# Kernel tuning notes

Hardware: AMD Instinct MI355X
Metric: run time of the kernel (lower is better)

The kernel has to match this reference:

```python
import jax, jax.numpy as jnp
import numpy as np

IN_FEATURES = 4096
OUT_FEATURES = 4096


def fht(x):
    """Normalized fast Walsh-Hadamard transform along last axis (n = power of 2).
    Equals x @ H_n / sqrt(n); matches matmul_hadU(t)_cuda when had_K is None (K=1)."""
    n = x.shape[-1]
    orig_shape = x.shape
    x = x.reshape(-1, n)
    h = 1
    while h < n:
        x = x.reshape(-1, n // (2 * h), 2, h)
        a = x[:, :, 0, :]
        b = x[:, :, 1, :]
        x = jnp.stack([a + b, a - b], axis=2).reshape(-1, n)
        h *= 2
    scale = jnp.asarray(1.0 / np.sqrt(n), dtype=x.dtype)
    return (x * scale).reshape(orig_shape)


def decode_e8p(Qidxs, grid_abs):
    """E8P12-style decode: each 16-bit codeword -> 8 fp16 weights.
    Low 8 bits index a 256-entry table of 8 absolute values; high 8 bits are
    per-element sign flips. Returns dense W of shape [out, in]."""
    idx = Qidxs.astype(jnp.int32) & 0xFFFF            # [out, in/8]
    abs_vals = grid_abs[idx & 0xFF]                   # [out, in/8, 8]
    sbits = (idx[..., None] >> (8 + jnp.arange(8, dtype=jnp.int32))) & 1
    signs = (1 - 2 * sbits).astype(grid_abs.dtype)    # [out, in/8, 8] in {+1,-1}
    w = abs_vals * signs
    return w.reshape(Qidxs.shape[0], -1)              # [out, in]


def setup_inputs() -> dict:
    key = jax.random.key(0)
    k1, k2, k3, k4, k5, k6 = jax.random.split(key, 6)
    inp = {}
    inp["input"] = jax.random.normal(k1, (2, 4096, IN_FEATURES), dtype=jnp.float16)
    inp["Qidxs"] = jax.random.randint(k2, (OUT_FEATURES, IN_FEATURES // 8), 0, 65536, dtype=jnp.int32)
    # abs half-integer-ish grid values (E8 lattice magnitudes live in ~[0.25, 3.75])
    inp["grid_abs"] = (jax.random.uniform(k3, (256, 8), dtype=jnp.float32) * 3.0 + 0.25).astype(jnp.float16)
    # SU/SV are random sign vectors in QuIP
    inp["SU"] = (1 - 2 * jax.random.bernoulli(k4, 0.5, (IN_FEATURES,)).astype(jnp.float16))
    inp["SV"] = (1 - 2 * jax.random.bernoulli(k5, 0.5, (OUT_FEATURES,)).astype(jnp.float16))
    inp["Wscale"] = jnp.ones((), dtype=jnp.float32)
    inp["bias"] = jax.random.normal(k6, (OUT_FEATURES,), dtype=jnp.float16) * jnp.float16(0.01)
    return inp


def reference(input, Qidxs, grid_abs, SU, SV, Wscale, bias):
    x = input.reshape(-1, input.shape[-1])            # [T, in]
    x = x * SU                                        # input sign rescale
    x = fht(x)                                        # H^T x / sqrt(n) (H symmetric)
    x = (x * Wscale).astype(jnp.float16)              # global weight scale
    W = decode_e8p(Qidxs, grid_abs)                   # [out, in] dequantized lattice weights
    out = jnp.dot(x, W.T, preferred_element_type=jnp.float32).astype(jnp.float16)  # [T, out]
    out = fht(out)                                    # output Hadamard
    out = out * SV + bias                             # output sign rescale + bias
    return out.reshape(*input.shape[:-1], out.shape[-1])
```

## Files before the change

### kernel.cpp

```cpp
#include <hip/hip_runtime.h>
#include <hip/hip_bf16.h>
#include <stdint.h>

typedef _Float16 f16;
typedef _Float16 f16x8 __attribute__((ext_vector_type(8)));
typedef float f32x4 __attribute__((ext_vector_type(4)));

#define N_FEAT 4096
#define M_ROWS 8192
#define QSTRIDE 512

#define GLD16(gptr, lptr)                                                      \
  __builtin_amdgcn_global_load_lds(                                            \
      (const __attribute__((address_space(1))) void*)(gptr),                   \
      (__attribute__((address_space(3))) void*)(uint32_t)(uintptr_t)(lptr),    \
      16, 0, 0)

#define PADI(i) ((i) + ((i) >> 4))

__device__ __forceinline__ void fht16(float v[16]) {
#pragma unroll
  for (int h = 1; h < 16; h <<= 1) {
#pragma unroll
    for (int i = 0; i < 16; i += (h << 1)) {
#pragma unroll
      for (int j = 0; j < h; ++j) {
        float a = v[i + j], b = v[i + j + h];
        v[i + j] = a + b;
        v[i + j + h] = a - b;
      }
    }
  }
}

__global__ __launch_bounds__(256) void k_fht_in(const float* __restrict__ x,
                                                const float* __restrict__ SU,
                                                const float* __restrict__ wscale,
                                                f16* __restrict__ out) {
  __shared__ float lds[4096 + 256];
  const int row = blockIdx.x;
  const int t = threadIdx.x;
  const float* xr = x + (size_t)row * N_FEAT;
  float v[16];

#pragma unroll
  for (int j = 0; j < 16; ++j) {
    int i = (j << 8) + t;
    v[j] = xr[i] * SU[i];
  }
  fht16(v);
#pragma unroll
  for (int j = 0; j < 16; ++j) lds[PADI((j << 8) + t)] = v[j];
  __syncthreads();

  const int a = t & 15, b = t >> 4;
#pragma unroll
  for (int j = 0; j < 16; ++j) v[j] = lds[PADI((b << 8) + (j << 4) + a)];
  fht16(v);
#pragma unroll
  for (int j = 0; j < 16; ++j) lds[PADI((b << 8) + (j << 4) + a)] = v[j];
  __syncthreads();

#pragma unroll
  for (int j = 0; j < 16; ++j) v[j] = lds[PADI((t << 4) + j)];
  fht16(v);
  const float s = wscale[0] * 0.015625f;
  f16* op = out + (size_t)row * N_FEAT + (t << 4);
  f16x8 o0, o1;
#pragma unroll
  for (int j = 0; j < 8; ++j) {
    o0[j] = (f16)(v[j] * s);
    o1[j] = (f16)(v[j + 8] * s);
  }
  *(f16x8*)(op) = o0;
  *(f16x8*)(op + 8) = o1;
}

__global__ __launch_bounds__(256) void k_decode(const int* __restrict__ q,
                                                const float* __restrict__ grid,
                                                int4* __restrict__ W) {
  __shared__ int4 tab[256];
  const int t = threadIdx.x;
  {
    const float4 g0 = *(const float4*)(grid + t * 8);
    const float4 g1 = *(const float4*)(grid + t * 8 + 4);
    union { f16 h[8]; int4 v; } u;
    u.h[0] = (f16)g0.x; u.h[1] = (f16)g0.y; u.h[2] = (f16)g0.z; u.h[3] = (f16)g0.w;
    u.h[4] = (f16)g1.x; u.h[5] = (f16)g1.y; u.h[6] = (f16)g1.z; u.h[7] = (f16)g1.w;
    tab[t] = u.v;
  }
  __syncthreads();
  const size_t idx = (size_t)blockIdx.x * 256 + t;
  const unsigned c = (unsigned)q[idx] & 0xffffu;
  int4 e = tab[c & 255u];
  e.x ^= (int)((((c >> 8) & 1u) << 15) | (((c >> 9) & 1u) << 31));
  e.y ^= (int)((((c >> 10) & 1u) << 15) | (((c >> 11) & 1u) << 31));
  e.z ^= (int)((((c >> 12) & 1u) << 15) | (((c >> 13) & 1u) << 31));
  e.w ^= (int)((((c >> 14) & 1u) << 15) | (((c >> 15) & 1u) << 31));
  W[idx] = e;
}

#define BM 128
#define BN 128
#define BK 64
#define KDIM 4096

__global__ __launch_bounds__(256) void k_gemm(const f16* __restrict__ A,
                                              const f16* __restrict__ B,
                                              f16* __restrict__ C) {
  __shared__ __attribute__((aligned(16))) f16 sA[BM * BK];
  __shared__ __attribute__((aligned(16))) f16 sB[BN * BK];
  const int tid = threadIdx.x;
  const int lane = tid & 63;
  const int w = tid >> 6;
  const int wr = w >> 1, wc = w & 1;
  const int m0 = blockIdx.y * BM;
  const int n0 = blockIdx.x * BN;

  f32x4 acc[4][4];
#pragma unroll
  for (int i = 0; i < 4; ++i)
#pragma unroll
    for (int j = 0; j < 4; ++j) acc[i][j] = (f32x4)0.0f;

  const int srow = lane >> 3;
  const int scc = lane & 7;
  const int quad = lane >> 4;
  const int ml = lane & 15;

  for (int k0 = 0; k0 < KDIM; k0 += BK) {
#pragma unroll
    for (int i = 0; i < 4; ++i) {
      const int rb = ((w << 2) + i) << 3;
      const int r = rb + srow;
      const int kc = scc ^ (r & 7);
      GLD16(A + (size_t)(m0 + r) * KDIM + k0 + (kc << 3), &sA[rb << 6]);
    }
#pragma unroll
    for (int i = 0; i < 4; ++i) {
      const int rb = ((w << 2) + i) << 3;
      const int r = rb + srow;
      const int kc = scc ^ (r & 7);
      GLD16(B + (size_t)(n0 + r) * KDIM + k0 + (kc << 3), &sB[rb << 6]);
    }
    __syncthreads();

#pragma unroll
    for (int s = 0; s < 2; ++s) {
      f16x8 af[4], bfr[4];
#pragma unroll
      for (int i = 0; i < 4; ++i) {
        const int m = (wr << 6) + (i << 4) + ml;
        const int kc = ((s << 2) + quad) ^ (m & 7);
        af[i] = *(const f16x8*)&sA[(m << 6) + (kc << 3)];
      }
#pragma unroll
      for (int j = 0; j < 4; ++j) {
        const int n = (wc << 6) + (j << 4) + ml;
        const int kc = ((s << 2) + quad) ^ (n & 7);
        bfr[j] = *(const f16x8*)&sB[(n << 6) + (kc << 3)];
      }
#pragma unroll
      for (int i = 0; i < 4; ++i)
#pragma unroll
        for (int j = 0; j < 4; ++j)
          acc[i][j] = __builtin_amdgcn_mfma_f32_16x16x32_f16(af[i], bfr[j],
                                                             acc[i][j], 0, 0, 0);
    }
    __syncthreads();
  }

#pragma unroll
  for (int i = 0; i < 4; ++i) {
#pragma unroll
    for (int j = 0; j < 4; ++j) {
      const int col = n0 + (wc << 6) + (j << 4) + ml;
      const int rowb = m0 + (wr << 6) + (i << 4) + (quad << 2);
#pragma unroll
      for (int r = 0; r < 4; ++r)
        C[(size_t)(rowb + r) * N_FEAT + col] = (f16)acc[i][j][r];
    }
  }
}

__global__ __launch_bounds__(256) void k_fht_out(const f16* __restrict__ Cin,
                                                 const float* __restrict__ SV,
                                                 const float* __restrict__ bias,
                                                 float* __restrict__ out) {
  __shared__ float lds[4096 + 256];
  const int row = blockIdx.x;
  const int t = threadIdx.x;
  const f16* xr = Cin + (size_t)row * N_FEAT;
  float v[16];

#pragma unroll
  for (int j = 0; j < 16; ++j) v[j] = (float)xr[(j << 8) + t];
  fht16(v);
#pragma unroll
  for (int j = 0; j < 16; ++j) lds[PADI((j << 8) + t)] = v[j];
  __syncthreads();

  const int a = t & 15, b = t >> 4;
#pragma unroll
  for (int j = 0; j < 16; ++j) v[j] = lds[PADI((b << 8) + (j << 4) + a)];
  fht16(v);
#pragma unroll
  for (int j = 0; j < 16; ++j) lds[PADI((b << 8) + (j << 4) + a)] = v[j];
  __syncthreads();

#pragma unroll
  for (int j = 0; j < 16; ++j) v[j] = lds[PADI((t << 4) + j)];
  fht16(v);
  float* op = out + (size_t)row * N_FEAT + (t << 4);
  float o[16];
#pragma unroll
  for (int j = 0; j < 16; ++j) {
    int i0 = (t << 4) + j;
    o[j] = v[j] * 0.015625f * SV[i0] + bias[i0];
  }
#pragma unroll
  for (int j = 0; j < 4; ++j)
    *(float4*)(op + 4 * j) = make_float4(o[4 * j], o[4 * j + 1],
                                         o[4 * j + 2], o[4 * j + 3]);
}

extern "C" void kernel_launch(void* const* d_in, const int* in_sizes, int n_in,
                              void* d_out, int out_size, void* d_ws, size_t ws_size,
                              hipStream_t stream) {
  const float* input = nullptr;
  const int* qidxs = nullptr;
  const float* grid_abs = nullptr;
  const float* wscale = nullptr;
  const float* v4k[3] = {nullptr, nullptr, nullptr};
  int n4 = 0;
  for (int i = 0; i < n_in; ++i) {
    switch (in_sizes[i]) {
      case 33554432: input = (const float*)d_in[i]; break;
      case 2097152:  qidxs = (const int*)d_in[i]; break;
      case 2048:     grid_abs = (const float*)d_in[i]; break;
      case 1:        wscale = (const float*)d_in[i]; break;
      case 4096:     if (n4 < 3) v4k[n4++] = (const float*)d_in[i]; break;
      default: break;
    }
  }
  const float* SU = v4k[0];
  const float* SV = v4k[1];
  const float* bias = v4k[2];

  f16* x = (f16*)d_out;
  f16* W = (f16*)((char*)d_out + (size_t)M_ROWS * N_FEAT * 2);
  f16* Cb = (f16*)d_ws;
  float* out = (float*)d_out;

  k_fht_in<<<M_ROWS, 256, 0, stream>>>(input, SU, wscale, x);
  k_decode<<<(N_FEAT * QSTRIDE) / 256, 256, 0, stream>>>(qidxs, grid_abs,
                                                         (int4*)W);
  dim3 g(N_FEAT / BN, M_ROWS / BM);
  k_gemm<<<g, 256, 0, stream>>>(x, W, Cb);
  k_fht_out<<<M_ROWS, 256, 0, stream>>>(Cb, SV, bias, out);
}
```

Measured before the change: 595.4 us.

## Fold output Hadamard into dequantized weights and fuse SV/bias into GEMM epilogue

```diff
diff --git a/kernel.cpp b/kernel.cpp
--- a/kernel.cpp
+++ b/kernel.cpp
@@ -16,7 +16,7 @@
       (__attribute__((address_space(3))) void*)(uint32_t)(uintptr_t)(lptr),    \
       16, 0, 0)
 
-#define PADI(i) ((i) + ((i) >> 4))
+#define PAD64(i) ((i) + (((i) >> 6) << 2))
 
 __device__ __forceinline__ void fht16(float v[16]) {
 #pragma unroll
@@ -31,6 +31,11 @@
       }
     }
   }
+}
+
+__device__ __forceinline__ void fht4(float& a, float& b, float& c, float& d) {
+  float t0 = a + b, t1 = a - b, t2 = c + d, t3 = c - d;
+  a = t0 + t2; b = t1 + t3; c = t0 - t2; d = t1 - t3;
 }
 
 __global__ __launch_bounds__(256) void k_fht_in(const float* __restrict__ x,
@@ -44,60 +49,148 @@
   float v[16];
 
 #pragma unroll
-  for (int j = 0; j < 16; ++j) {
-    int i = (j << 8) + t;
-    v[j] = xr[i] * SU[i];
+  for (int j = 0; j < 4; ++j) {
+    const float4 a = *(const float4*)(xr + (t << 4) + 4 * j);
+    const float4 s = *(const float4*)(SU + (t << 4) + 4 * j);
+    v[4 * j + 0] = a.x * s.x; v[4 * j + 1] = a.y * s.y;
+    v[4 * j + 2] = a.z * s.z; v[4 * j + 3] = a.w * s.w;
   }
   fht16(v);
 #pragma unroll
-  for (int j = 0; j < 16; ++j) lds[PADI((j << 8) + t)] = v[j];
+  for (int j = 0; j < 4; ++j)
+    *(float4*)&lds[PAD64((t << 4) + 4 * j)] =
+        make_float4(v[4 * j], v[4 * j + 1], v[4 * j + 2], v[4 * j + 3]);
   __syncthreads();
 
   const int a = t & 15, b = t >> 4;
 #pragma unroll
-  for (int j = 0; j < 16; ++j) v[j] = lds[PADI((b << 8) + (j << 4) + a)];
+  for (int j = 0; j < 16; ++j) v[j] = lds[PAD64((b << 8) + (j << 4) + a)];
   fht16(v);
 #pragma unroll
-  for (int j = 0; j < 16; ++j) lds[PADI((b << 8) + (j << 4) + a)] = v[j];
-  __syncthreads();
-
-#pragma unroll
-  for (int j = 0; j < 16; ++j) v[j] = lds[PADI((t << 4) + j)];
+  for (int j = 0; j < 16; ++j) lds[PAD64((b << 8) + (j << 4) + a)] = v[j];
+  __syncthreads();
+
+#pragma unroll
+  for (int j = 0; j < 16; ++j) v[j] = lds[PAD64((j << 8) + t)];
   fht16(v);
   const float s = wscale[0] * 0.015625f;
-  f16* op = out + (size_t)row * N_FEAT + (t << 4);
-  f16x8 o0, o1;
-#pragma unroll
-  for (int j = 0; j < 8; ++j) {
-    o0[j] = (f16)(v[j] * s);
-    o1[j] = (f16)(v[j + 8] * s);
-  }
-  *(f16x8*)(op) = o0;
-  *(f16x8*)(op + 8) = o1;
-}
-
-__global__ __launch_bounds__(256) void k_decode(const int* __restrict__ q,
-                                                const float* __restrict__ grid,
-                                                int4* __restrict__ W) {
-  __shared__ int4 tab[256];
+  f16* op = out + (size_t)row * N_FEAT;
+#pragma unroll
+  for (int j = 0; j < 16; ++j) op[(j << 8) + t] = (f16)(v[j] * s);
+}
+
+__global__ __launch_bounds__(256) void k_wA(const int* __restrict__ q,
+                                            const float* __restrict__ grid,
+                                            f16* __restrict__ Wp) {
+  __shared__ float tabf[2048];
+  __shared__ float tile[64 * 65];
   const int t = threadIdx.x;
-  {
-    const float4 g0 = *(const float4*)(grid + t * 8);
-    const float4 g1 = *(const float4*)(grid + t * 8 + 4);
-    union { f16 h[8]; int4 v; } u;
-    u.h[0] = (f16)g0.x; u.h[1] = (f16)g0.y; u.h[2] = (f16)g0.z; u.h[3] = (f16)g0.w;
-    u.h[4] = (f16)g1.x; u.h[5] = (f16)g1.y; u.h[6] = (f16)g1.z; u.h[7] = (f16)g1.w;
-    tab[t] = u.v;
-  }
-  __syncthreads();
-  const size_t idx = (size_t)blockIdx.x * 256 + t;
-  const unsigned c = (unsigned)q[idx] & 0xffffu;
-  int4 e = tab[c & 255u];
-  e.x ^= (int)((((c >> 8) & 1u) << 15) | (((c >> 9) & 1u) << 31));
-  e.y ^= (int)((((c >> 10) & 1u) << 15) | (((c >> 11) & 1u) << 31));
-  e.z ^= (int)((((c >> 12) & 1u) << 15) | (((c >> 13) & 1u) << 31));
-  e.w ^= (int)((((c >> 14) & 1u) << 15) | (((c >> 15) & 1u) << 31));
-  W[idx] = e;
+  const int kg = blockIdx.x;
+  const int ng = blockIdx.y;
+  {
+    *(float4*)&tabf[t * 8] = *(const float4*)(grid + t * 8);
+    *(float4*)&tabf[t * 8 + 4] = *(const float4*)(grid + t * 8 + 4);
+  }
+  __syncthreads();
+
+#pragma unroll
+  for (int e2 = 0; e2 < 2; ++e2) {
+    const int e = t + (e2 << 8);
+    const int nl = e >> 3, c = e & 7;
+    const unsigned code =
+        (unsigned)q[(size_t)(ng * 64 + nl) * QSTRIDE + kg * 8 + c] & 0xffffu;
+    const float* tb = &tabf[(code & 255u) * 8];
+#pragma unroll
+    for (int j = 0; j < 8; ++j) {
+      const int bi = __float_as_int(tb[j]) ^ (int)(((code >> (8 + j)) & 1u) << 31);
+      tile[nl * 65 + (c << 3) + j] = __int_as_float(bi);
+    }
+  }
+  __syncthreads();
+
+  {
+    const int k = t & 63, p = t >> 6;
+    float v[16];
+#pragma unroll
+    for (int j = 0; j < 16; ++j) v[j] = tile[(16 * p + j) * 65 + k];
+    fht16(v);
+#pragma unroll
+    for (int j = 0; j < 16; ++j) tile[(16 * p + j) * 65 + k] = v[j];
+  }
+  __syncthreads();
+
+  {
+    const int k = t & 63, base = (t >> 6) << 2;
+#pragma unroll
+    for (int bb = 0; bb < 4; ++bb) {
+      const int low = base + bb;
+      float v0 = tile[(low) * 65 + k],      v1 = tile[(low + 16) * 65 + k];
+      float v2 = tile[(low + 32) * 65 + k], v3 = tile[(low + 48) * 65 + k];
+      fht4(v0, v1, v2, v3);
+      tile[(low) * 65 + k] = v0;      tile[(low + 16) * 65 + k] = v1;
+      tile[(low + 32) * 65 + k] = v2; tile[(low + 48) * 65 + k] = v3;
+    }
+  }
+  __syncthreads();
+
+  {
+    const int nl = t >> 2, koff = (t & 3) << 4;
+    union { f16 h[16]; int4 v[2]; } u;
+#pragma unroll
+    for (int i = 0; i < 16; ++i) u.h[i] = (f16)tile[nl * 65 + koff + i];
+    int4* dst = (int4*)(Wp + (size_t)(ng * 64 + nl) * N_FEAT + kg * 64 + koff);
+    dst[0] = u.v[0];
+    dst[1] = u.v[1];
+  }
+}
+
+__global__ __launch_bounds__(256) void k_wB(f16* __restrict__ Wp) {
+  __shared__ float tile[64 * 65];
+  const int t = threadIdx.x;
+  const int kg = blockIdx.x;
+  const int n0 = blockIdx.y;
+  {
+    const int n1 = t >> 2, koff = (t & 3) << 4;
+    const f16* src = Wp + (size_t)(n0 + 64 * n1) * N_FEAT + kg * 64 + koff;
+    union { f16 h[16]; int4 v[2]; } u;
+    u.v[0] = ((const int4*)src)[0];
+    u.v[1] = ((const int4*)src)[1];
+#pragma unroll
+    for (int i = 0; i < 16; ++i) tile[n1 * 65 + koff + i] = (float)u.h[i];
+  }
+  __syncthreads();
+  {
+    const int k = t & 63, p = t >> 6;
+    float v[16];
+#pragma unroll
+    for (int j = 0; j < 16; ++j) v[j] = tile[(16 * p + j) * 65 + k];
+    fht16(v);
+#pragma unroll
+    for (int j = 0; j < 16; ++j) tile[(16 * p + j) * 65 + k] = v[j];
+  }
+  __syncthreads();
+  {
+    const int k = t & 63, base = (t >> 6) << 2;
+#pragma unroll
+    for (int bb = 0; bb < 4; ++bb) {
+      const int low = base + bb;
+      float v0 = tile[(low) * 65 + k],      v1 = tile[(low + 16) * 65 + k];
+      float v2 = tile[(low + 32) * 65 + k], v3 = tile[(low + 48) * 65 + k];
+      fht4(v0, v1, v2, v3);
+      tile[(low) * 65 + k] = v0;      tile[(low + 16) * 65 + k] = v1;
+      tile[(low + 32) * 65 + k] = v2; tile[(low + 48) * 65 + k] = v3;
+    }
+  }
+  __syncthreads();
+  {
+    const int n1 = t >> 2, koff = (t & 3) << 4;
+    union { f16 h[16]; int4 v[2]; } u;
+#pragma unroll
+    for (int i = 0; i < 16; ++i) u.h[i] = (f16)tile[n1 * 65 + koff + i];
+    int4* dst = (int4*)(Wp + (size_t)(n0 + 64 * n1) * N_FEAT + kg * 64 + koff);
+    dst[0] = u.v[0];
+    dst[1] = u.v[1];
+  }
 }
 
 #define BM 128
@@ -107,7 +200,9 @@
 
 __global__ __launch_bounds__(256) void k_gemm(const f16* __restrict__ A,
                                               const f16* __restrict__ B,
-                                              f16* __restrict__ C) {
+                                              float* __restrict__ C,
+                                              const float* __restrict__ SV,
+                                              const float* __restrict__ bias) {
   __shared__ __attribute__((aligned(16))) f16 sA[BM * BK];
   __shared__ __attribute__((aligned(16))) f16 sB[BN * BK];
   const int tid = threadIdx.x;
@@ -171,57 +266,18 @@
   }
 
 #pragma unroll
-  for (int i = 0; i < 4; ++i) {
-#pragma unroll
-    for (int j = 0; j < 4; ++j) {
-      const int col = n0 + (wc << 6) + (j << 4) + ml;
+  for (int j = 0; j < 4; ++j) {
+    const int col = n0 + (wc << 6) + (j << 4) + ml;
+    const float sv = SV[col] * 0.015625f;
+    const float bs = bias[col];
+#pragma unroll
+    for (int i = 0; i < 4; ++i) {
       const int rowb = m0 + (wr << 6) + (i << 4) + (quad << 2);
 #pragma unroll
       for (int r = 0; r < 4; ++r)
-        C[(size_t)(rowb + r) * N_FEAT + col] = (f16)acc[i][j][r];
-    }
-  }
-}
-
-__global__ __launch_bounds__(256) void k_fht_out(const f16* __restrict__ Cin,
-                                                 const float* __restrict__ SV,
-                                                 const float* __restrict__ bias,
-                                                 float* __restrict__ out) {
-  __shared__ float lds[4096 + 256];
-  const int row = blockIdx.x;
-  const int t = threadIdx.x;
-  const f16* xr = Cin + (size_t)row * N_FEAT;
-  float v[16];
-
-#pragma unroll
-  for (int j = 0; j < 16; ++j) v[j] = (float)xr[(j << 8) + t];
-  fht16(v);
-#pragma unroll
-  for (int j = 0; j < 16; ++j) lds[PADI((j << 8) + t)] = v[j];
-  __syncthreads();
-
-  const int a = t & 15, b = t >> 4;
-#pragma unroll
-  for (int j = 0; j < 16; ++j) v[j] = lds[PADI((b << 8) + (j << 4) + a)];
-  fht16(v);
-#pragma unroll
-  for (int j = 0; j < 16; ++j) lds[PADI((b << 8) + (j << 4) + a)] = v[j];
-  __syncthreads();
-
-#pragma unroll
-  for (int j = 0; j < 16; ++j) v[j] = lds[PADI((t << 4) + j)];
-  fht16(v);
-  float* op = out + (size_t)row * N_FEAT + (t << 4);
-  float o[16];
-#pragma unroll
-  for (int j = 0; j < 16; ++j) {
-    int i0 = (t << 4) + j;
-    o[j] = v[j] * 0.015625f * SV[i0] + bias[i0];
-  }
-#pragma unroll
-  for (int j = 0; j < 4; ++j)
-    *(float4*)(op + 4 * j) = make_float4(o[4 * j], o[4 * j + 1],
-                                         o[4 * j + 2], o[4 * j + 3]);
+        C[(size_t)(rowb + r) * N_FEAT + col] = acc[i][j][r] * sv + bs;
+    }
+  }
 }
 
 extern "C" void kernel_launch(void* const* d_in, const int* in_sizes, int n_in,
@@ -247,15 +303,14 @@
   const float* SV = v4k[1];
   const float* bias = v4k[2];
 
-  f16* x = (f16*)d_out;
-  f16* W = (f16*)((char*)d_out + (size_t)M_ROWS * N_FEAT * 2);
-  f16* Cb = (f16*)d_ws;
+  f16* x = (f16*)d_ws;
+  f16* Wp = (f16*)const_cast<float*>(input);
   float* out = (float*)d_out;
 
   k_fht_in<<<M_ROWS, 256, 0, stream>>>(input, SU, wscale, x);
-  k_decode<<<(N_FEAT * QSTRIDE) / 256, 256, 0, stream>>>(qidxs, grid_abs,
-                                                         (int4*)W);
+  dim3 gw(64, 64);
+  k_wA<<<gw, 256, 0, stream>>>(qidxs, grid_abs, Wp);
+  k_wB<<<gw, 256, 0, stream>>>(Wp);
   dim3 g(N_FEAT / BN, M_ROWS / BM);
-  k_gemm<<<g, 256, 0, stream>>>(x, W, Cb);
-  k_fht_out<<<M_ROWS, 256, 0, stream>>>(Cb, SV, bias, out);
-}
+  k_gemm<<<g, 256, 0, stream>>>(x, Wp, out, SV, bias);
+}
```

After: 556.8 us. 6.5% less time.
